# Performance work log

Measured on AMD Instinct MI355X. Metric: run time of the kernel, lower is better.

The kernel has to match this reference:

```python
import jax, jax.numpy as jnp
import numpy as np

TAU = 0.1
MASK_VAL = 1e9


def setup_inputs() -> dict:
    key = jax.random.key(0)
    ka, kb = jax.random.split(key)
    B, D = 4096, 512
    return {
        "view_a": jax.random.normal(ka, (B, D), dtype=jnp.float32),
        "view_b": jax.random.normal(kb, (B, D), dtype=jnp.float32),
    }


def _l2norm(x):
    return x / jnp.maximum(jnp.linalg.norm(x, axis=-1, keepdims=True), 1e-12)


def reference(view_a, view_b):
    a = _l2norm(view_a)
    b = _l2norm(view_b)
    B = a.shape[0]
    labels = jnp.arange(B)  # start_i = 0 (single device)
    mask = jnp.eye(B, dtype=a.dtype) * MASK_VAL

    logits_aa = a @ a.T / TAU - mask
    logits_bb = b @ b.T / TAU - mask
    logits_ab = a @ b.T / TAU
    logits_ba = b @ a.T / TAU

    full_a = jnp.concatenate([logits_ab, logits_aa], axis=1)  # [B, 2B]
    full_b = jnp.concatenate([logits_ba, logits_bb], axis=1)

    def ce(logits):
        logp = jax.nn.log_softmax(logits, axis=-1)
        return -jnp.mean(jnp.take_along_axis(logp, labels[:, None], axis=-1))

    loss = (ce(full_a) + ce(full_b)) / 2

    pred = jnp.argmax(full_a, axis=-1)
    acc = 100.0 * jnp.sum(pred == labels) / B
    return loss, acc
```

## Files before the change

### kernel.cpp

```cpp
#include <hip/hip_runtime.h>
#include <stdint.h>


#define BN 4096
#define DK 512
#define NEG_BIG -1e30f
#define SCL 0.15625f
#define SCL2 0.225396744f
#define C2 14.4269504f
#define TILE_BYTES (64 * DK)
#define NRS 16
#define NBLK 544

typedef __attribute__((ext_vector_type(16))) float floatx16;
typedef __attribute__((ext_vector_type(8))) int intx8;

__global__ void __launch_bounds__(256) prep_kernel(
    const float* __restrict__ A, const float* __restrict__ Bv,
    unsigned char* __restrict__ Gn, float* __restrict__ diag,
    float* __restrict__ out, float* __restrict__ zbase,
    float* __restrict__ mbase) {
  const int gtid = blockIdx.x * 256 + threadIdx.x;
  if (gtid < 2) out[gtid] = 0.0f;
  for (int idx = gtid; idx < (NRS + 64) * 8192; idx += 1024 * 256)
    zbase[idx] = 0.0f;
  for (int idx = gtid; idx < (NRS + 32) * 4096; idx += 1024 * 256)
    mbase[idx] = NEG_BIG;

  const int w = threadIdx.x >> 6, lane = threadIdx.x & 63;
  const int row = blockIdx.x * 4 + w;
  const float4* pa4 = (const float4*)(A + (size_t)row * DK);
  const float4* pb4 = (const float4*)(Bv + (size_t)row * DK);
  float4 a0 = pa4[lane * 2], a1 = pa4[lane * 2 + 1];
  float4 b0 = pb4[lane * 2], b1 = pb4[lane * 2 + 1];
  float ssa = a0.x * a0.x + a0.y * a0.y + a0.z * a0.z + a0.w * a0.w +
              a1.x * a1.x + a1.y * a1.y + a1.z * a1.z + a1.w * a1.w;
  float ssb = b0.x * b0.x + b0.y * b0.y + b0.z * b0.z + b0.w * b0.w +
              b1.x * b1.x + b1.y * b1.y + b1.z * b1.z + b1.w * b1.w;
  float sab = a0.x * b0.x + a0.y * b0.y + a0.z * b0.z + a0.w * b0.w +
              a1.x * b1.x + a1.y * b1.y + a1.z * b1.z + a1.w * b1.w;
#pragma unroll
  for (int off = 32; off > 0; off >>= 1) {
    ssa += __shfl_xor(ssa, off);
    ssb += __shfl_xor(ssb, off);
    sab += __shfl_xor(sab, off);
  }
  float na = fmaxf(sqrtf(ssa), 1e-12f);
  float nb = fmaxf(sqrtf(ssb), 1e-12f);
  const float s = 8.0f;
  float sa = s / na, sb = s / nb;
  const int doff = (lane >> 2) * 32 + (lane & 1) * 16 + ((lane >> 1) & 1) * 8;
  {
    int v0 = __builtin_amdgcn_cvt_pk_fp8_f32(a0.x * sa, a0.y * sa, 0, false);
    v0 = __builtin_amdgcn_cvt_pk_fp8_f32(a0.z * sa, a0.w * sa, v0, true);
    int v1 = __builtin_amdgcn_cvt_pk_fp8_f32(a1.x * sa, a1.y * sa, 0, false);
    v1 = __builtin_amdgcn_cvt_pk_fp8_f32(a1.z * sa, a1.w * sa, v1, true);
    int2 pv; pv.x = v0; pv.y = v1;
    *(int2*)(Gn + (size_t)row * DK + doff) = pv;
  }
  {
    int v0 = __builtin_amdgcn_cvt_pk_fp8_f32(b0.x * sb, b0.y * sb, 0, false);
    v0 = __builtin_amdgcn_cvt_pk_fp8_f32(b0.z * sb, b0.w * sb, v0, true);
    int v1 = __builtin_amdgcn_cvt_pk_fp8_f32(b1.x * sb, b1.y * sb, 0, false);
    v1 = __builtin_amdgcn_cvt_pk_fp8_f32(b1.z * sb, b1.w * sb, v1, true);
    int2 pv; pv.x = v0; pv.y = v1;
    *(int2*)(Gn + (size_t)(BN + row) * DK + doff) = pv;
  }
  if (lane == 0) diag[row] = (sab / (na * nb)) * 10.0f;
}

__global__ void __launch_bounds__(256, 2) tiles_kernel(
    const unsigned char* __restrict__ Gn,
    float* __restrict__ pRS, float* __restrict__ pCS,
    float* __restrict__ pRM, float* __restrict__ pCM) {
  __shared__ __align__(16) unsigned char smem[TILE_BYTES + 2048];

  int bid = blockIdx.x, I = 0;
  for (;;) {
    const int nc = (135 - 2 * I) >> 3;
    if (bid < nc) break;
    bid -= nc; ++I;
  }
  const int chunk = bid;
  const int j0 = 2 * I + chunk * 8;
  const int ntiles = min(8, 128 - 2 * I - chunk * 8);

  const int tid = threadIdx.x;
  const int lane = tid & 63, w = tid >> 6;
  const int n5 = lane & 31, h = lane >> 5;
  const int rbase = I * 128 + w * 32;

  intx8 aw[8];
  {
    const unsigned char* p = Gn + (size_t)(rbase + n5) * DK + h * 16;
#pragma unroll
    for (int i = 0; i < 8; ++i) {
      int4 c0 = *(const int4*)(p + i * 64);
      int4 c1 = *(const int4*)(p + i * 64 + 32);
      intx8 v = {c0.x, c0.y, c0.z, c0.w, c1.x, c1.y, c1.z, c1.w};
      aw[i] = v;
    }
  }

  auto stage = [&](int j) {
    const int cb = j * 64;
#pragma unroll
    for (int ii = 0; ii < 8; ++ii) {
      const int cp = w * 8 + ii;
      const int cl = cp * 2 + h;
      const unsigned char* src =
          Gn + (size_t)(cb + cl) * DK + ((n5 ^ (cl & 31)) * 16);
      __builtin_amdgcn_global_load_lds(
          (const __attribute__((address_space(1))) void*)src,
          (__attribute__((address_space(3))) void*)(smem + cp * 1024),
          16, 0, 0);
    }
  };

  float l[16], mxr[16];
#pragma unroll
  for (int r = 0; r < 16; ++r) { l[r] = 0.f; mxr[r] = NEG_BIG; }

  float* T = (float*)(smem + TILE_BYTES);

#pragma unroll 1
  for (int t = 0; t < ntiles; ++t) {
    const int j = j0 + t;
    stage(j);
    __syncthreads();

    floatx16 acc[2];
#pragma unroll
    for (int cs = 0; cs < 2; ++cs)
#pragma unroll
      for (int r = 0; r < 16; ++r) acc[cs][r] = 0.f;

    const unsigned char* bbase = smem + (size_t)n5 * DK;
#pragma unroll
    for (int i = 0; i < 8; ++i) {
      const int p1 = ((4 * i + h) ^ n5) * 16;
      const int p2 = ((4 * i + 2 + h) ^ n5) * 16;
#pragma unroll
      for (int cs = 0; cs < 2; ++cs) {
        int4 b0 = *(const int4*)(bbase + cs * 32 * DK + p1);
        int4 b1 = *(const int4*)(bbase + cs * 32 * DK + p2);
        intx8 bw = {b0.x, b0.y, b0.z, b0.w, b1.x, b1.y, b1.z, b1.w};
        acc[cs] = __builtin_amdgcn_mfma_scale_f32_32x32x64_f8f6f4(
            aw[i], bw, acc[cs], 0, 0, 0, 0x7F7F7F7F, 0, 0x7F7F7F7F);
      }
    }

    const int cbase = j * 64;
    const bool diagp = ((j >> 1) == I);
    const bool lblp = (I < 32) && (j >= 64);
    const int colg0 = cbase + n5, colg1 = cbase + 32 + n5;
    float csum0 = 0.f, csum1 = 0.f, cmax0 = NEG_BIG, cmax1 = NEG_BIG;

#define EPI_BODY(EXCL0_EXPR, EXCL1_EXPR)                                    \
  _Pragma("unroll")                                                         \
  for (int r = 0; r < 16; ++r) {                                            \
    const int rowg = rbase + (r & 3) + 8 * (r >> 2) + 4 * h;                \
    (void)rowg;                                                             \
    {                                                                       \
      const float v = acc[0][r];                                            \
      const bool excl = (EXCL0_EXPR);                                       \
      const float e = excl ? 0.f : exp2f(fmaf(v, SCL2, -C2));               \
      const float vm = excl ? NEG_BIG : v;                                  \
      l[r] += e; mxr[r] = fmaxf(mxr[r], vm);                                \
      csum0 += e; cmax0 = fmaxf(cmax0, vm);                                 \
    }                                                                       \
    {                                                                       \
      const float v = acc[1][r];                                            \
      const bool excl = (EXCL1_EXPR);                                       \
      const float e = excl ? 0.f : exp2f(fmaf(v, SCL2, -C2));               \
      const float vm = excl ? NEG_BIG : v;                                  \
      l[r] += e; mxr[r] = fmaxf(mxr[r], vm);                                \
      csum1 += e; cmax1 = fmaxf(cmax1, vm);                                 \
    }                                                                       \
  }

    if (diagp) {
      EPI_BODY(colg0 <= rowg, colg1 <= rowg)
    } else if (lblp) {
      EPI_BODY(colg0 == rowg + BN, colg1 == rowg + BN)
    } else {
      EPI_BODY(false, false)
    }
#undef EPI_BODY

    csum0 += __shfl_xor(csum0, 32);
    csum1 += __shfl_xor(csum1, 32);
    cmax0 = fmaxf(cmax0, __shfl_xor(cmax0, 32));
    cmax1 = fmaxf(cmax1, __shfl_xor(cmax1, 32));
    float* cps = T;
    float* cpm = T + 256;
    if (h == 0) {
      cps[w * 64 + n5] = csum0; cps[w * 64 + 32 + n5] = csum1;
      cpm[w * 64 + n5] = cmax0; cpm[w * 64 + 32 + n5] = cmax1;
    }
    __syncthreads();
    if (tid < 64) {
      const float s =
          cps[tid] + cps[64 + tid] + cps[128 + tid] + cps[192 + tid];
      pCS[(size_t)I * 8192 + cbase + tid] = s;
      if (j < 64) {
        const float m = fmaxf(fmaxf(cpm[tid], cpm[64 + tid]),
                              fmaxf(cpm[128 + tid], cpm[192 + tid]));
        pCM[(size_t)I * 4096 + cbase + tid] = m;
      }
    }
  }

#pragma unroll
  for (int off = 1; off < 32; off <<= 1)
#pragma unroll
    for (int r = 0; r < 16; ++r) l[r] += __shfl_xor(l[r], off);
  if (I < 32) {
#pragma unroll
    for (int off = 1; off < 32; off <<= 1)
#pragma unroll
      for (int r = 0; r < 16; ++r)
        mxr[r] = fmaxf(mxr[r], __shfl_xor(mxr[r], off));
  }
  if (n5 == 0) {
#pragma unroll
    for (int r = 0; r < 16; ++r) {
      const int rowg = rbase + (r & 3) + 8 * (r >> 2) + 4 * h;
      pRS[(size_t)chunk * 8192 + rowg] = l[r];
      if (I < 32) pRM[(size_t)chunk * 4096 + rowg] = mxr[r];
    }
  }
}

__global__ void __launch_bounds__(256) finalize_kernel(
    const float* __restrict__ pRS, const float* __restrict__ pCS,
    const float* __restrict__ pRM, const float* __restrict__ pCM,
    const float* __restrict__ diag, float* __restrict__ out) {
  const int k = threadIdx.x & 7;
  const int r = threadIdx.x >> 3;
  const int i = blockIdx.x * 32 + r;

  float SA = 0.f, SB = 0.f, MA = NEG_BIG;
#pragma unroll
  for (int q = 0; q < 2; ++q) {
    const int s = k * 2 + q;
    SA += pRS[(size_t)s * 8192 + i];
    SB += pRS[(size_t)s * 8192 + BN + i];
    MA = fmaxf(MA, pRM[(size_t)s * 4096 + i]);
  }
#pragma unroll
  for (int q = 0; q < 8; ++q) {
    const int s = k * 8 + q;
    SA += pCS[(size_t)s * 8192 + i];
    SB += pCS[(size_t)s * 8192 + BN + i];
  }
#pragma unroll
  for (int q = 0; q < 4; ++q) {
    const int s = k * 4 + q;
    MA = fmaxf(MA, pCM[(size_t)s * 4096 + i]);
  }
#pragma unroll
  for (int off = 1; off < 8; off <<= 1) {
    SA += __shfl_xor(SA, off);
    SB += __shfl_xor(SB, off);
    MA = fmaxf(MA, __shfl_xor(MA, off));
  }

  float lossi = 0.f, corr = 0.f;
  if (k == 0) {
    const float d = diag[i];
    const float eL = exp2f(fmaf(d, 1.44269504f, -C2));
    lossi = (10.0f + logf(SA + eL) - d) + (10.0f + logf(SB + eL) - d);
    corr = (d >= MA * SCL) ? 1.f : 0.f;
  }
#pragma unroll
  for (int off = 32; off > 0; off >>= 1) {
    lossi += __shfl_xor(lossi, off);
    corr += __shfl_xor(corr, off);
  }
  __shared__ float sred[2][4];
  if ((threadIdx.x & 63) == 0) {
    int w = threadIdx.x >> 6;
    sred[0][w] = lossi; sred[1][w] = corr;
  }
  __syncthreads();
  if (threadIdx.x == 0) {
    float ls = sred[0][0] + sred[0][1] + sred[0][2] + sred[0][3];
    float cs = sred[1][0] + sred[1][1] + sred[1][2] + sred[1][3];
    atomicAdd(&out[0], ls * (1.0f / 8192.0f));
    atomicAdd(&out[1], cs * (100.0f / 4096.0f));
  }
}

extern "C" void kernel_launch(void* const* d_in, const int* in_sizes, int n_in,
                              void* d_out, int out_size, void* d_ws, size_t ws_size,
                              hipStream_t stream) {
  const float* A = (const float*)d_in[0];
  const float* Bv = (const float*)d_in[1];
  unsigned char* Gn = (unsigned char*)d_ws;
  float* diag = (float*)(Gn + (size_t)8192 * DK);
  float* pRS = diag + BN;
  float* pCS = pRS + NRS * 8192;
  float* pRM = pCS + 64 * 8192;
  float* pCM = pRM + NRS * 4096;
  float* out = (float*)d_out;

  prep_kernel<<<BN / 4, 256, 0, stream>>>(A, Bv, Gn, diag, out, pRS, pRM);
  tiles_kernel<<<NBLK, 256, 0, stream>>>(Gn, pRS, pCS, pRM, pCM);
  finalize_kernel<<<BN / 32, 256, 0, stream>>>(pRS, pCS, pRM, pCM, diag, out);
}
```

Before: 116.5 us.

## Load B tiles directly from global and defer column reductions past the tile loop

Removes the LDS staging of each 64-column B tile; every wave now reads its B fragments straight from global memory (L2/L1) into registers for the MFMA. Per-tile column partial sums and maxima are written to per-tile LDS slots and reduced once after the loop. This drops both per-tile __syncthreads barriers and the cross-half shuffles. The cost is redundant global loads of the same B data by all four waves, with no swizzled LDS reuse, so performance now depends on cache bandwidth and latency hiding.

```diff
diff --git a/kernel.cpp b/kernel.cpp
--- a/kernel.cpp
+++ b/kernel.cpp
@@ -8,7 +8,6 @@
 #define SCL 0.15625f
 #define SCL2 0.225396744f
 #define C2 14.4269504f
-#define TILE_BYTES (64 * DK)
 #define NRS 16
 #define NBLK 544
 
@@ -73,7 +72,8 @@
     const unsigned char* __restrict__ Gn,
     float* __restrict__ pRS, float* __restrict__ pCS,
     float* __restrict__ pRM, float* __restrict__ pCM) {
-  __shared__ __align__(16) unsigned char smem[TILE_BYTES + 2048];
+  __shared__ float cps[8][8][64];
+  __shared__ float cpm[8][8][64];
 
   int bid = blockIdx.x, I = 0;
   for (;;) {
@@ -89,6 +89,7 @@
   const int lane = tid & 63, w = tid >> 6;
   const int n5 = lane & 31, h = lane >> 5;
   const int rbase = I * 128 + w * 32;
+  const int w2h = w * 2 + h;
 
   intx8 aw[8];
   {
@@ -102,32 +103,14 @@
     }
   }
 
-  auto stage = [&](int j) {
-    const int cb = j * 64;
-#pragma unroll
-    for (int ii = 0; ii < 8; ++ii) {
-      const int cp = w * 8 + ii;
-      const int cl = cp * 2 + h;
-      const unsigned char* src =
-          Gn + (size_t)(cb + cl) * DK + ((n5 ^ (cl & 31)) * 16);
-      __builtin_amdgcn_global_load_lds(
-          (const __attribute__((address_space(1))) void*)src,
-          (__attribute__((address_space(3))) void*)(smem + cp * 1024),
-          16, 0, 0);
-    }
-  };
-
   float l[16], mxr[16];
 #pragma unroll
   for (int r = 0; r < 16; ++r) { l[r] = 0.f; mxr[r] = NEG_BIG; }
-
-  float* T = (float*)(smem + TILE_BYTES);
 
 #pragma unroll 1
   for (int t = 0; t < ntiles; ++t) {
     const int j = j0 + t;
-    stage(j);
-    __syncthreads();
+    const int cbase = j * 64;
 
     floatx16 acc[2];
 #pragma unroll
@@ -135,22 +118,22 @@
 #pragma unroll
       for (int r = 0; r < 16; ++r) acc[cs][r] = 0.f;
 
-    const unsigned char* bbase = smem + (size_t)n5 * DK;
-#pragma unroll
+    const unsigned char* pb0 = Gn + (size_t)(cbase + n5) * DK + h * 16;
+    const unsigned char* pb1 = pb0 + (size_t)32 * DK;
+#pragma unroll 2
     for (int i = 0; i < 8; ++i) {
-      const int p1 = ((4 * i + h) ^ n5) * 16;
-      const int p2 = ((4 * i + 2 + h) ^ n5) * 16;
-#pragma unroll
-      for (int cs = 0; cs < 2; ++cs) {
-        int4 b0 = *(const int4*)(bbase + cs * 32 * DK + p1);
-        int4 b1 = *(const int4*)(bbase + cs * 32 * DK + p2);
-        intx8 bw = {b0.x, b0.y, b0.z, b0.w, b1.x, b1.y, b1.z, b1.w};
-        acc[cs] = __builtin_amdgcn_mfma_scale_f32_32x32x64_f8f6f4(
-            aw[i], bw, acc[cs], 0, 0, 0, 0x7F7F7F7F, 0, 0x7F7F7F7F);
-      }
-    }
-
-    const int cbase = j * 64;
+      int4 b0 = *(const int4*)(pb0 + i * 64);
+      int4 b1 = *(const int4*)(pb0 + i * 64 + 32);
+      intx8 bw = {b0.x, b0.y, b0.z, b0.w, b1.x, b1.y, b1.z, b1.w};
+      acc[0] = __builtin_amdgcn_mfma_scale_f32_32x32x64_f8f6f4(
+          aw[i], bw, acc[0], 0, 0, 0, 0x7F7F7F7F, 0, 0x7F7F7F7F);
+      int4 c0 = *(const int4*)(pb1 + i * 64);
+      int4 c1 = *(const int4*)(pb1 + i * 64 + 32);
+      intx8 cw = {c0.x, c0.y, c0.z, c0.w, c1.x, c1.y, c1.z, c1.w};
+      acc[1] = __builtin_amdgcn_mfma_scale_f32_32x32x64_f8f6f4(
+          aw[i], cw, acc[1], 0, 0, 0, 0x7F7F7F7F, 0, 0x7F7F7F7F);
+    }
+
     const bool diagp = ((j >> 1) == I);
     const bool lblp = (I < 32) && (j >= 64);
     const int colg0 = cbase + n5, colg1 = cbase + 32 + n5;
@@ -188,26 +171,25 @@
     }
 #undef EPI_BODY
 
-    csum0 += __shfl_xor(csum0, 32);
-    csum1 += __shfl_xor(csum1, 32);
-    cmax0 = fmaxf(cmax0, __shfl_xor(cmax0, 32));
-    cmax1 = fmaxf(cmax1, __shfl_xor(cmax1, 32));
-    float* cps = T;
-    float* cpm = T + 256;
-    if (h == 0) {
-      cps[w * 64 + n5] = csum0; cps[w * 64 + 32 + n5] = csum1;
-      cpm[w * 64 + n5] = cmax0; cpm[w * 64 + 32 + n5] = cmax1;
-    }
-    __syncthreads();
-    if (tid < 64) {
-      const float s =
-          cps[tid] + cps[64 + tid] + cps[128 + tid] + cps[192 + tid];
-      pCS[(size_t)I * 8192 + cbase + tid] = s;
-      if (j < 64) {
-        const float m = fmaxf(fmaxf(cpm[tid], cpm[64 + tid]),
-                              fmaxf(cpm[128 + tid], cpm[192 + tid]));
-        pCM[(size_t)I * 4096 + cbase + tid] = m;
-      }
+    cps[t][w2h][n5] = csum0;
+    cps[t][w2h][32 + n5] = csum1;
+    cpm[t][w2h][n5] = cmax0;
+    cpm[t][w2h][32 + n5] = cmax1;
+  }
+
+  __syncthreads();
+  for (int idx = tid; idx < ntiles * 64; idx += 256) {
+    const int t = idx >> 6, col = idx & 63;
+    const int j = j0 + t;
+    float s = 0.f;
+#pragma unroll
+    for (int q = 0; q < 8; ++q) s += cps[t][q][col];
+    pCS[(size_t)I * 8192 + j * 64 + col] = s;
+    if (j < 64) {
+      float m = cpm[t][0][col];
+#pragma unroll
+      for (int q = 1; q < 8; ++q) m = fmaxf(m, cpm[t][q][col]);
+      pCM[(size_t)I * 4096 + j * 64 + col] = m;
     }
   }
 
```

Result: slower. 222.0 us (+90.5%).

## Use 256-row 512-thread tiles and skip unneeded max tracking in epilogue

Applied to the files above, without the earlier changes.

Each block of the symmetric-Gram tiles kernel now covers 256 rows with 8 waves, up from 128 rows with 4 waves. Every column tile staged into LDS is therefore reused by twice as many rows, and each block does a fixed 4 tiles, so the grid becomes 528 uniform blocks. The epilogue is specialised so row and column max tracking only runs where it feeds the accuracy argmax (A rows, first half of the columns). The partial-buffer counts, the prep zero/max init and the finalize reduction strides change to match. The cost is more registers and occupancy pressure per block, plus a 16-way LDS column reduction done by a single wave.

```diff
diff --git a/kernel.cpp b/kernel.cpp
--- a/kernel.cpp
+++ b/kernel.cpp
@@ -9,8 +9,9 @@
 #define SCL2 0.225396744f
 #define C2 14.4269504f
 #define TILE_BYTES (64 * DK)
-#define NRS 16
-#define NBLK 544
+#define NRS 32
+#define NCS 32
+#define NBLK 528
 
 typedef __attribute__((ext_vector_type(16))) float floatx16;
 typedef __attribute__((ext_vector_type(8))) int intx8;
@@ -22,9 +23,9 @@
     float* __restrict__ mbase) {
   const int gtid = blockIdx.x * 256 + threadIdx.x;
   if (gtid < 2) out[gtid] = 0.0f;
-  for (int idx = gtid; idx < (NRS + 64) * 8192; idx += 1024 * 256)
+  for (int idx = gtid; idx < (NRS + NCS) * 8192; idx += 1024 * 256)
     zbase[idx] = 0.0f;
-  for (int idx = gtid; idx < (NRS + 32) * 4096; idx += 1024 * 256)
+  for (int idx = gtid; idx < 64 * 4096; idx += 1024 * 256)
     mbase[idx] = NEG_BIG;
 
   const int w = threadIdx.x >> 6, lane = threadIdx.x & 63;
@@ -69,26 +70,29 @@
   if (lane == 0) diag[row] = (sab / (na * nb)) * 10.0f;
 }
 
-__global__ void __launch_bounds__(256, 2) tiles_kernel(
+__global__ void __launch_bounds__(512, 2) tiles_kernel(
     const unsigned char* __restrict__ Gn,
     float* __restrict__ pRS, float* __restrict__ pCS,
     float* __restrict__ pRM, float* __restrict__ pCM) {
-  __shared__ __align__(16) unsigned char smem[TILE_BYTES + 2048];
+  __shared__ __align__(16) unsigned char smem[TILE_BYTES];
+  __shared__ float cps[16][64];
+  __shared__ float cpm[16][64];
 
   int bid = blockIdx.x, I = 0;
   for (;;) {
-    const int nc = (135 - 2 * I) >> 3;
+    const int nc = 32 - I;
     if (bid < nc) break;
     bid -= nc; ++I;
   }
   const int chunk = bid;
-  const int j0 = 2 * I + chunk * 8;
-  const int ntiles = min(8, 128 - 2 * I - chunk * 8);
+  const int j0 = 4 * I + chunk * 4;
 
   const int tid = threadIdx.x;
   const int lane = tid & 63, w = tid >> 6;
   const int n5 = lane & 31, h = lane >> 5;
-  const int rbase = I * 128 + w * 32;
+  const int rbase = I * 256 + w * 32;
+  const int w2h = w * 2 + h;
+  const bool arows = (I < 16);
 
   intx8 aw[8];
   {
@@ -105,8 +109,8 @@
   auto stage = [&](int j) {
     const int cb = j * 64;
 #pragma unroll
-    for (int ii = 0; ii < 8; ++ii) {
-      const int cp = w * 8 + ii;
+    for (int ii = 0; ii < 4; ++ii) {
+      const int cp = w * 4 + ii;
       const int cl = cp * 2 + h;
       const unsigned char* src =
           Gn + (size_t)(cb + cl) * DK + ((n5 ^ (cl & 31)) * 16);
@@ -121,10 +125,8 @@
 #pragma unroll
   for (int r = 0; r < 16; ++r) { l[r] = 0.f; mxr[r] = NEG_BIG; }
 
-  float* T = (float*)(smem + TILE_BYTES);
-
 #pragma unroll 1
-  for (int t = 0; t < ntiles; ++t) {
+  for (int t = 0; t < 4; ++t) {
     const int j = j0 + t;
     stage(j);
     __syncthreads();
@@ -151,12 +153,13 @@
     }
 
     const int cbase = j * 64;
-    const bool diagp = ((j >> 1) == I);
-    const bool lblp = (I < 32) && (j >= 64);
+    const bool diagp = ((j >> 2) == I);
+    const bool lblp = arows && ((j >> 2) == 16 + I);
+    const bool docmax = (j < 64);
     const int colg0 = cbase + n5, colg1 = cbase + 32 + n5;
     float csum0 = 0.f, csum1 = 0.f, cmax0 = NEG_BIG, cmax1 = NEG_BIG;
 
-#define EPI_BODY(EXCL0_EXPR, EXCL1_EXPR)                                    \
+#define EPI_BODY(EXCL0_EXPR, EXCL1_EXPR, DO_R, DO_C)                        \
   _Pragma("unroll")                                                         \
   for (int r = 0; r < 16; ++r) {                                            \
     const int rowg = rbase + (r & 3) + 8 * (r >> 2) + 4 * h;                \
@@ -165,47 +168,55 @@
       const float v = acc[0][r];                                            \
       const bool excl = (EXCL0_EXPR);                                       \
       const float e = excl ? 0.f : exp2f(fmaf(v, SCL2, -C2));               \
-      const float vm = excl ? NEG_BIG : v;                                  \
-      l[r] += e; mxr[r] = fmaxf(mxr[r], vm);                                \
-      csum0 += e; cmax0 = fmaxf(cmax0, vm);                                 \
+      l[r] += e; csum0 += e;                                                \
+      if (DO_R || DO_C) {                                                   \
+        const float vm = excl ? NEG_BIG : v;                                \
+        if (DO_R) mxr[r] = fmaxf(mxr[r], vm);                               \
+        if (DO_C) cmax0 = fmaxf(cmax0, vm);                                 \
+      }                                                                     \
     }                                                                       \
     {                                                                       \
       const float v = acc[1][r];                                            \
       const bool excl = (EXCL1_EXPR);                                       \
       const float e = excl ? 0.f : exp2f(fmaf(v, SCL2, -C2));               \
-      const float vm = excl ? NEG_BIG : v;                                  \
-      l[r] += e; mxr[r] = fmaxf(mxr[r], vm);                                \
-      csum1 += e; cmax1 = fmaxf(cmax1, vm);                                 \
+      l[r] += e; csum1 += e;                                                \
+      if (DO_R || DO_C) {                                                   \
+        const float vm = excl ? NEG_BIG : v;                                \
+        if (DO_R) mxr[r] = fmaxf(mxr[r], vm);                               \
+        if (DO_C) cmax1 = fmaxf(cmax1, vm);                                 \
+      }                                                                     \
     }                                                                       \
   }
 
     if (diagp) {
-      EPI_BODY(colg0 <= rowg, colg1 <= rowg)
+      if (arows) { EPI_BODY(colg0 <= rowg, colg1 <= rowg, true, true) }
+      else       { EPI_BODY(colg0 <= rowg, colg1 <= rowg, false, false) }
     } else if (lblp) {
-      EPI_BODY(colg0 == rowg + BN, colg1 == rowg + BN)
+      EPI_BODY(colg0 == rowg + BN, colg1 == rowg + BN, true, false)
+    } else if (arows) {
+      if (docmax) { EPI_BODY(false, false, true, true) }
+      else        { EPI_BODY(false, false, true, false) }
     } else {
-      EPI_BODY(false, false)
+      EPI_BODY(false, false, false, false)
     }
 #undef EPI_BODY
 
-    csum0 += __shfl_xor(csum0, 32);
-    csum1 += __shfl_xor(csum1, 32);
-    cmax0 = fmaxf(cmax0, __shfl_xor(cmax0, 32));
-    cmax1 = fmaxf(cmax1, __shfl_xor(cmax1, 32));
-    float* cps = T;
-    float* cpm = T + 256;
-    if (h == 0) {
-      cps[w * 64 + n5] = csum0; cps[w * 64 + 32 + n5] = csum1;
-      cpm[w * 64 + n5] = cmax0; cpm[w * 64 + 32 + n5] = cmax1;
+    cps[w2h][n5] = csum0;
+    cps[w2h][32 + n5] = csum1;
+    if (docmax) {
+      cpm[w2h][n5] = cmax0;
+      cpm[w2h][32 + n5] = cmax1;
     }
     __syncthreads();
     if (tid < 64) {
-      const float s =
-          cps[tid] + cps[64 + tid] + cps[128 + tid] + cps[192 + tid];
+      float s = 0.f;
+#pragma unroll
+      for (int q = 0; q < 16; ++q) s += cps[q][tid];
       pCS[(size_t)I * 8192 + cbase + tid] = s;
-      if (j < 64) {
-        const float m = fmaxf(fmaxf(cpm[tid], cpm[64 + tid]),
-                              fmaxf(cpm[128 + tid], cpm[192 + tid]));
+      if (docmax) {
+        float m = cpm[0][tid];
+#pragma unroll
+        for (int q = 1; q < 16; ++q) m = fmaxf(m, cpm[q][tid]);
         pCM[(size_t)I * 4096 + cbase + tid] = m;
       }
     }
@@ -215,7 +226,7 @@
   for (int off = 1; off < 32; off <<= 1)
 #pragma unroll
     for (int r = 0; r < 16; ++r) l[r] += __shfl_xor(l[r], off);
-  if (I < 32) {
+  if (arows) {
 #pragma unroll
     for (int off = 1; off < 32; off <<= 1)
 #pragma unroll
@@ -227,7 +238,7 @@
     for (int r = 0; r < 16; ++r) {
       const int rowg = rbase + (r & 3) + 8 * (r >> 2) + 4 * h;
       pRS[(size_t)chunk * 8192 + rowg] = l[r];
-      if (I < 32) pRM[(size_t)chunk * 4096 + rowg] = mxr[r];
+      if (arows) pRM[(size_t)chunk * 4096 + rowg] = mxr[r];
     }
   }
 }
@@ -242,21 +253,21 @@
 
   float SA = 0.f, SB = 0.f, MA = NEG_BIG;
 #pragma unroll
-  for (int q = 0; q < 2; ++q) {
-    const int s = k * 2 + q;
+  for (int q = 0; q < 4; ++q) {
+    const int s = k * 4 + q;
     SA += pRS[(size_t)s * 8192 + i];
     SB += pRS[(size_t)s * 8192 + BN + i];
     MA = fmaxf(MA, pRM[(size_t)s * 4096 + i]);
   }
 #pragma unroll
-  for (int q = 0; q < 8; ++q) {
-    const int s = k * 8 + q;
+  for (int q = 0; q < 4; ++q) {
+    const int s = k * 4 + q;
     SA += pCS[(size_t)s * 8192 + i];
     SB += pCS[(size_t)s * 8192 + BN + i];
   }
 #pragma unroll
-  for (int q = 0; q < 4; ++q) {
-    const int s = k * 4 + q;
+  for (int q = 0; q < 2; ++q) {
+    const int s = k * 2 + q;
     MA = fmaxf(MA, pCM[(size_t)s * 4096 + i]);
   }
 #pragma unroll
@@ -301,11 +312,11 @@
   float* diag = (float*)(Gn + (size_t)8192 * DK);
   float* pRS = diag + BN;
   float* pCS = pRS + NRS * 8192;
-  float* pRM = pCS + 64 * 8192;
-  float* pCM = pRM + NRS * 4096;
+  float* pRM = pCS + NCS * 8192;
+  float* pCM = pRM + 32 * 4096;
   float* out = (float*)d_out;
 
   prep_kernel<<<BN / 4, 256, 0, stream>>>(A, Bv, Gn, diag, out, pRS, pRM);
-  tiles_kernel<<<NBLK, 256, 0, stream>>>(Gn, pRS, pCS, pRM, pCM);
+  tiles_kernel<<<NBLK, 512, 0, stream>>>(Gn, pRS, pCS, pRM, pCM);
   finalize_kernel<<<BN / 32, 256, 0, stream>>>(pRS, pCS, pRM, pCM, diag, out);
 }
```

Measured after the change: 136.1 us. 16.8% more time.
